# Kernel tuning notes

Measured on AMD Instinct MI355X. Metric: run time of the kernel, lower is better.

The kernel has to match this reference:

```python
import jax, jax.numpy as jnp
import numpy as np

N, IN_CH, OUT_CH, E = 100000, 256, 8, 6400000

def setup_inputs() -> dict:
    key = jax.random.key(0)
    k1, k2, k3, k4 = jax.random.split(key, 4)
    X = jax.random.normal(k1, (N, IN_CH), dtype=jnp.float32)
    edge_index = jax.random.randint(k2, (2, E), 0, N, dtype=jnp.int64)
    # torch Linear weights: [out_channels, in_channels], no bias
    W1 = jax.random.normal(k3, (OUT_CH, IN_CH), dtype=jnp.float32) / np.sqrt(IN_CH)
    W2 = jax.random.normal(k4, (OUT_CH, IN_CH), dtype=jnp.float32) / np.sqrt(IN_CH)
    return {"X": X, "edge_index": edge_index, "W1": W1, "W2": W2}

def reference(X, edge_index, W1, W2):
    # Project first ([N, out] is tiny), then gather -- same math as
    # W1(X[e0]) + W2(X[e1]) but avoids two [E, in_channels] intermediates.
    P1 = X @ W1.T  # [N, out]
    P2 = X @ W2.T  # [N, out]
    return P1[edge_index[0]] + P2[edge_index[1]]  # [E, out]
```

## Files before the change

### kernel.cpp

```cpp
#include <hip/hip_runtime.h>
#include <hip/hip_fp16.h>

#define IN_CH 256
#define OUT_CH 8
#define RB 4

typedef float f32x4 __attribute__((ext_vector_type(4)));

__device__ __forceinline__ unsigned pack2h(float a, float b) {
    __half2 h = __floats2half2_rn(a, b);
    return *(unsigned*)&h;
}

__global__ __launch_bounds__(256) void proj_kernel(
    const float* __restrict__ X,
    const float4* __restrict__ W1v,
    const float4* __restrict__ W2v,
    __half* __restrict__ P1h,
    __half* __restrict__ P2h,
    int n, int nwaves)
{
    const int lane  = threadIdx.x & 63;
    const int gwave = (blockIdx.x * 256 + threadIdx.x) >> 6;

    float4 w[16];
    #pragma unroll
    for (int o = 0; o < 8; ++o) {
        w[o]     = W1v[o * 64 + lane];
        w[8 + o] = W2v[o * 64 + lane];
    }

    const int g      = (lane >> 2) & 15;
    const bool owner = (lane & 3) == 0;

    for (int r0 = gwave * RB; r0 < n; r0 += nwaves * RB) {
        float4 x[RB];
        #pragma unroll
        for (int b = 0; b < RB; ++b) {
            const int r = r0 + b;
            if (r < n)
                x[b] = *(const float4*)(X + (size_t)r * IN_CH + lane * 4);
        }

        #pragma unroll
        for (int b = 0; b < RB; ++b) {
            const int r = r0 + b;
            if (r >= n) break;

            float acc[16];
            #pragma unroll
            for (int o = 0; o < 16; ++o) {
                const float4 ww = w[o];
                acc[o] = x[b].x * ww.x + x[b].y * ww.y
                       + x[b].z * ww.z + x[b].w * ww.w;
            }

            #pragma unroll
            for (int j = 0; j < 8; ++j) {
                float give = (lane & 32) ? acc[j] : acc[j + 8];
                float keep = (lane & 32) ? acc[j + 8] : acc[j];
                acc[j] = keep + __shfl_xor(give, 32, 64);
            }
            #pragma unroll
            for (int j = 0; j < 4; ++j) {
                float give = (lane & 16) ? acc[j] : acc[j + 4];
                float keep = (lane & 16) ? acc[j + 4] : acc[j];
                acc[j] = keep + __shfl_xor(give, 16, 64);
            }
            #pragma unroll
            for (int j = 0; j < 2; ++j) {
                float give = (lane & 8) ? acc[j] : acc[j + 2];
                float keep = (lane & 8) ? acc[j + 2] : acc[j];
                acc[j] = keep + __shfl_xor(give, 8, 64);
            }
            {
                float give = (lane & 4) ? acc[0] : acc[1];
                float keep = (lane & 4) ? acc[1] : acc[0];
                acc[0] = keep + __shfl_xor(give, 4, 64);
            }
            float a = acc[0];
            a += __shfl_xor(a, 1, 64);
            a += __shfl_xor(a, 2, 64);

            if (owner) {
                __half h = __float2half(a);
                __half* dst = (g < 8)
                    ? (P1h + (size_t)r * OUT_CH + g)
                    : (P2h + (size_t)r * OUT_CH + (g - 8));
                *dst = h;
            }
        }
    }
}

__device__ __forceinline__ void addh8(const uint4 a, const uint4 b,
                                      f32x4& r0, f32x4& r1) {
    const __half2* ah = (const __half2*)&a;
    const __half2* bh = (const __half2*)&b;
    float2 s0 = __half22float2(ah[0]);
    float2 s1 = __half22float2(ah[1]);
    float2 s2 = __half22float2(ah[2]);
    float2 s3 = __half22float2(ah[3]);
    float2 t0 = __half22float2(bh[0]);
    float2 t1 = __half22float2(bh[1]);
    float2 t2 = __half22float2(bh[2]);
    float2 t3 = __half22float2(bh[3]);
    r0 = (f32x4){ s0.x + t0.x, s0.y + t0.y, s1.x + t1.x, s1.y + t1.y };
    r1 = (f32x4){ s2.x + t2.x, s2.y + t2.y, s3.x + t3.x, s3.y + t3.y };
}

__global__ __launch_bounds__(256) void gather_kernel(
    const int* __restrict__ e0,
    const int* __restrict__ e1,
    const uint4* __restrict__ T1,
    const uint4* __restrict__ T2,
    f32x4* __restrict__ outv,
    int E, int n)
{
    const int tid  = threadIdx.x;
    const int base = blockIdx.x * 1024;
    const unsigned nmax = (unsigned)(n - 1);

    if (base + 1024 <= E) {
        unsigned i0[4], i1[4];
        #pragma unroll
        for (int k = 0; k < 4; ++k) {
            const int ek = base + k * 256 + tid;
            i0[k] = (unsigned)__builtin_nontemporal_load(e0 + ek);
            i1[k] = (unsigned)__builtin_nontemporal_load(e1 + ek);
        }
        uint4 a[4], b[4];
        #pragma unroll
        for (int k = 0; k < 4; ++k) {
            a[k] = T1[i0[k] > nmax ? nmax : i0[k]];
            b[k] = T2[i1[k] > nmax ? nmax : i1[k]];
        }
        #pragma unroll
        for (int k = 0; k < 4; ++k) {
            f32x4 r0, r1;
            addh8(a[k], b[k], r0, r1);
            const size_t oi = 2u * (size_t)(base + k * 256 + tid);
            __builtin_nontemporal_store(r0, outv + oi);
            __builtin_nontemporal_store(r1, outv + oi + 1);
        }
    } else {
        for (int k = 0; k < 4; ++k) {
            const int ek = base + k * 256 + tid;
            if (ek >= E) break;
            unsigned i0 = (unsigned)__builtin_nontemporal_load(e0 + ek);
            unsigned i1 = (unsigned)__builtin_nontemporal_load(e1 + ek);
            uint4 a = T1[i0 > nmax ? nmax : i0];
            uint4 b = T2[i1 > nmax ? nmax : i1];
            f32x4 r0, r1;
            addh8(a, b, r0, r1);
            const size_t oi = 2u * (size_t)ek;
            __builtin_nontemporal_store(r0, outv + oi);
            __builtin_nontemporal_store(r1, outv + oi + 1);
        }
    }
}

extern "C" void kernel_launch(void* const* d_in, const int* in_sizes, int n_in,
                              void* d_out, int out_size, void* d_ws, size_t ws_size,
                              hipStream_t stream) {
    const float* X    = (const float*)d_in[0];
    const int*   eidx = (const int*)d_in[1];
    const float* W1   = (const float*)d_in[2];
    const float* W2   = (const float*)d_in[3];

    const int n = in_sizes[0] / IN_CH;
    const int E = in_sizes[1] / 2;

    __half* P1h = (__half*)d_ws;
    __half* P2h = P1h + (size_t)n * OUT_CH;

    const int proj_blocks = 1024;
    const int nwaves = proj_blocks * 4;
    proj_kernel<<<proj_blocks, 256, 0, stream>>>(
        X, (const float4*)W1, (const float4*)W2, P1h, P2h, n, nwaves);

    const int gather_blocks = (E + 1023) / 1024;
    gather_kernel<<<gather_blocks, 256, 0, stream>>>(
        eidx, eidx + E, (const uint4*)P1h, (const uint4*)P2h,
        (f32x4*)d_out, E, n);
}
```

Measured before the change: 135.6 us.

## Compute projection with bf16 MFMA via per-wave LDS tiles instead of shuffle reductions

Replaces the shuffle-reduction dot-product projection with a per-wave 16-row tile staged through LDS as bf16, multiplied on the matrix cores with a 16x16x32 bf16 MFMA against all 16 output channels at once. This targets the many cross-lane shuffles and VALU work in the projection phase. It also lowers the projection grid from 1024 to 768 blocks. It adds LDS traffic, bf16 rounding of X and W (lower precision than fp32), and a dependency on correct MFMA operand layout.

```diff
diff --git a/kernel.cpp b/kernel.cpp
--- a/kernel.cpp
+++ b/kernel.cpp
@@ -3,91 +3,75 @@
 
 #define IN_CH 256
 #define OUT_CH 8
-#define RB 4
+#define LROW 264
 
-typedef float f32x4 __attribute__((ext_vector_type(4)));
+typedef float f32x4  __attribute__((ext_vector_type(4)));
+typedef short short8v __attribute__((ext_vector_type(8)));
+typedef short short4v __attribute__((ext_vector_type(4)));
 
-__device__ __forceinline__ unsigned pack2h(float a, float b) {
-    __half2 h = __floats2half2_rn(a, b);
-    return *(unsigned*)&h;
+__device__ __forceinline__ short f2bf(float f) {
+    unsigned u = __float_as_uint(f);
+    u += 0x7FFFu + ((u >> 16) & 1u);
+    return (short)(u >> 16);
 }
 
 __global__ __launch_bounds__(256) void proj_kernel(
     const float* __restrict__ X,
-    const float4* __restrict__ W1v,
-    const float4* __restrict__ W2v,
+    const float* __restrict__ W1,
+    const float* __restrict__ W2,
     __half* __restrict__ P1h,
     __half* __restrict__ P2h,
-    int n, int nwaves)
+    int n, int ntiles, int nwaves)
 {
-    const int lane  = threadIdx.x & 63;
-    const int gwave = (blockIdx.x * 256 + threadIdx.x) >> 6;
+    __shared__ short Xs[4][16][LROW];
 
-    float4 w[16];
+    const int wv   = threadIdx.x >> 6;
+    const int lane = threadIdx.x & 63;
+    const int gw   = (blockIdx.x * 256 + threadIdx.x) >> 6;
+
+    const int o  = lane & 15;
+    const int lk = lane >> 4;
+
+    const float* wrow = (o < 8) ? (W1 + (size_t)o * IN_CH)
+                                : (W2 + (size_t)(o - 8) * IN_CH);
+    short8v bfr[8];
     #pragma unroll
-    for (int o = 0; o < 8; ++o) {
-        w[o]     = W1v[o * 64 + lane];
-        w[8 + o] = W2v[o * 64 + lane];
+    for (int kb = 0; kb < 8; ++kb) {
+        float4 u = *(const float4*)(wrow + kb * 32 + lk * 8);
+        float4 v = *(const float4*)(wrow + kb * 32 + lk * 8 + 4);
+        short8v b;
+        b[0] = f2bf(u.x); b[1] = f2bf(u.y); b[2] = f2bf(u.z); b[3] = f2bf(u.w);
+        b[4] = f2bf(v.x); b[5] = f2bf(v.y); b[6] = f2bf(v.z); b[7] = f2bf(v.w);
+        bfr[kb] = b;
     }
 
-    const int g      = (lane >> 2) & 15;
-    const bool owner = (lane & 3) == 0;
+    for (int t = gw; t < ntiles; t += nwaves) {
+        const int r0 = t * 16;
 
-    for (int r0 = gwave * RB; r0 < n; r0 += nwaves * RB) {
-        float4 x[RB];
         #pragma unroll
-        for (int b = 0; b < RB; ++b) {
-            const int r = r0 + b;
-            if (r < n)
-                x[b] = *(const float4*)(X + (size_t)r * IN_CH + lane * 4);
+        for (int i = 0; i < 16; ++i) {
+            float4 x = make_float4(0.f, 0.f, 0.f, 0.f);
+            if (r0 + i < n)
+                x = *(const float4*)(X + (size_t)(r0 + i) * IN_CH + lane * 4);
+            short4v s;
+            s[0] = f2bf(x.x); s[1] = f2bf(x.y); s[2] = f2bf(x.z); s[3] = f2bf(x.w);
+            *(short4v*)&Xs[wv][i][lane * 4] = s;
+        }
+
+        f32x4 acc = {0.f, 0.f, 0.f, 0.f};
+        #pragma unroll
+        for (int kb = 0; kb < 8; ++kb) {
+            short8v a = *(const short8v*)&Xs[wv][o][kb * 32 + lk * 8];
+            acc = __builtin_amdgcn_mfma_f32_16x16x32_bf16(a, bfr[kb], acc, 0, 0, 0);
         }
 
         #pragma unroll
-        for (int b = 0; b < RB; ++b) {
-            const int r = r0 + b;
-            if (r >= n) break;
-
-            float acc[16];
-            #pragma unroll
-            for (int o = 0; o < 16; ++o) {
-                const float4 ww = w[o];
-                acc[o] = x[b].x * ww.x + x[b].y * ww.y
-                       + x[b].z * ww.z + x[b].w * ww.w;
-            }
-
-            #pragma unroll
-            for (int j = 0; j < 8; ++j) {
-                float give = (lane & 32) ? acc[j] : acc[j + 8];
-                float keep = (lane & 32) ? acc[j + 8] : acc[j];
-                acc[j] = keep + __shfl_xor(give, 32, 64);
-            }
-            #pragma unroll
-            for (int j = 0; j < 4; ++j) {
-                float give = (lane & 16) ? acc[j] : acc[j + 4];
-                float keep = (lane & 16) ? acc[j + 4] : acc[j];
-                acc[j] = keep + __shfl_xor(give, 16, 64);
-            }
-            #pragma unroll
-            for (int j = 0; j < 2; ++j) {
-                float give = (lane & 8) ? acc[j] : acc[j + 2];
-                float keep = (lane & 8) ? acc[j + 2] : acc[j];
-                acc[j] = keep + __shfl_xor(give, 8, 64);
-            }
-            {
-                float give = (lane & 4) ? acc[0] : acc[1];
-                float keep = (lane & 4) ? acc[1] : acc[0];
-                acc[0] = keep + __shfl_xor(give, 4, 64);
-            }
-            float a = acc[0];
-            a += __shfl_xor(a, 1, 64);
-            a += __shfl_xor(a, 2, 64);
-
-            if (owner) {
-                __half h = __float2half(a);
-                __half* dst = (g < 8)
-                    ? (P1h + (size_t)r * OUT_CH + g)
-                    : (P2h + (size_t)r * OUT_CH + (g - 8));
-                *dst = h;
+        for (int r = 0; r < 4; ++r) {
+            const int row = r0 + lk * 4 + r;
+            if (row < n) {
+                __half h = __float2half(acc[r]);
+                if (o < 8) P1h[(size_t)row * OUT_CH + o] = h;
+                else       P2h[(size_t)row * OUT_CH + (o - 8)] = h;
             }
         }
     }
@@ -174,10 +158,11 @@
     __half* P1h = (__half*)d_ws;
     __half* P2h = P1h + (size_t)n * OUT_CH;
 
-    const int proj_blocks = 1024;
+    const int ntiles = (n + 15) / 16;
+    const int proj_blocks = 768;
     const int nwaves = proj_blocks * 4;
     proj_kernel<<<proj_blocks, 256, 0, stream>>>(
-        X, (const float4*)W1, (const float4*)W2, P1h, P2h, n, nwaves);
+        X, W1, W2, P1h, P2h, n, ntiles, nwaves);
 
     const int gather_blocks = (E + 1023) / 1024;
     gather_kernel<<<gather_blocks, 256, 0, stream>>>(
```

After: 137.3 us. No clear change (+1.2%).
